# Kernel tuning notes

Hardware: AMD Instinct MI355X
Metric: run time of the kernel (lower is better)

The kernel has to match this reference:

```python
import jax, jax.numpy as jnp
import numpy as np

OFFSET_FP32 = np.uint32(1064828928)  # L-mul exponent-bias correction constant for float32


def lmul_matmul(A, B):
    """Approximate A @ B (m,n)x(n,p) via integer-add-as-multiply on float bit patterns.

    Torch ref adds bit patterns in int64 then truncates with .to(torch.uint32),
    i.e. arithmetic mod 2**32 -- identical to plain uint32 wraparound addition,
    so we stay in uint32 and avoid needing x64 mode.
    """
    Au = jax.lax.bitcast_convert_type(A, jnp.uint32)          # (m, n)
    Bu = jax.lax.bitcast_convert_type(B, jnp.uint32)          # (n, p)
    prod_bits = Au[:, :, None] + Bu[None, :, :] - OFFSET_FP32  # (m, n, p), wraps mod 2^32
    prod = jax.lax.bitcast_convert_type(prod_bits, jnp.float32)
    return prod.sum(axis=1)                                    # (m, p)


def setup_inputs() -> dict:
    key = jax.random.key(0)
    k1, k2, k3 = jax.random.split(key, 3)
    m, n, p = 256, 512, 512
    x = jax.random.normal(k1, (m, n), dtype=jnp.float32)
    bound = 1.0 / np.sqrt(n)  # kaiming_uniform(a=sqrt(5)) -> U(-1/sqrt(fan_in), 1/sqrt(fan_in))
    weight = jax.random.uniform(k2, (p, n), dtype=jnp.float32, minval=-bound, maxval=bound)
    bias = jax.random.uniform(k3, (p,), dtype=jnp.float32, minval=-bound, maxval=bound)
    return {"x": x, "weight": weight, "bias": bias}


def reference(x, weight, bias):
    out = lmul_matmul(x, weight.T)
    return out + bias
```

## Files before the change

kernel.cpp:

```cpp
#include <hip/hip_runtime.h>
#include <stdint.h>


#define OFFSET_FP32 1064828928u

constexpr int M = 256;
constexpr int N = 512;
constexpr int P = 512;

constexpr int BM = 8;
constexpr int BP = 64;
constexpr int TM = 4;

__global__ __launch_bounds__(512) void lmul_linear_kernel(
    const uint32_t* __restrict__ xb,
    const uint32_t* __restrict__ wb,
    const float*    __restrict__ bias,
    float*          __restrict__ out)
{
    __shared__ uint32_t Bs[BP][N];
    __shared__ float    Red[4][BM][BP];

    const int tid  = threadIdx.x;
    const int lane = tid & 63;
    const int wq   = __builtin_amdgcn_readfirstlane(tid >> 6);
    const int ks   = wq & 3;
    const int mq   = wq >> 2;

    const int p0 = blockIdx.y * BP;
    const int m0 = blockIdx.x * BM + mq * TM;

    auto stage = [&](int h) {
        #pragma unroll
        for (int i = 0; i < 8; ++i) {
            const int row = wq * 8 + i;
            const uint32_t* src = wb + (size_t)(p0 + row) * N
                                + (size_t)(h * 64 + (lane ^ (row & 7))) * 4;
            uint32_t* dst = &Bs[row][h * 256];
            __builtin_amdgcn_global_load_lds(
                (const __attribute__((address_space(1))) uint32_t*)src,
                (__attribute__((address_space(3))) uint32_t*)dst,
                16, 0, 0);
        }
    };

    float acc[TM][4] = {};
    const int rot = lane & 7;

    const uint32_t* xr0 = xb + (size_t)(m0 + 0) * N;
    const uint32_t* xr1 = xb + (size_t)(m0 + 1) * N;
    const uint32_t* xr2 = xb + (size_t)(m0 + 2) * N;
    const uint32_t* xr3 = xb + (size_t)(m0 + 3) * N;

    auto compute = [&](int h) {
        const uint32_t* brow = &Bs[lane][(h * 64 + ks * 16) * 4];
        const int xoff = h * 256 + ks * 64;
        #pragma unroll 8
        for (int j = 0; j < 16; ++j) {
            const uint4 b  = *(const uint4*)&brow[(j ^ rot) * 4];
            const uint4 a0 = *(const uint4*)(xr0 + xoff + j * 4);
            const uint4 a1 = *(const uint4*)(xr1 + xoff + j * 4);
            const uint4 a2 = *(const uint4*)(xr2 + xoff + j * 4);
            const uint4 a3 = *(const uint4*)(xr3 + xoff + j * 4);
            acc[0][0] += __uint_as_float((a0.x - OFFSET_FP32) + b.x);
            acc[0][1] += __uint_as_float((a0.y - OFFSET_FP32) + b.y);
            acc[0][2] += __uint_as_float((a0.z - OFFSET_FP32) + b.z);
            acc[0][3] += __uint_as_float((a0.w - OFFSET_FP32) + b.w);
            acc[1][0] += __uint_as_float((a1.x - OFFSET_FP32) + b.x);
            acc[1][1] += __uint_as_float((a1.y - OFFSET_FP32) + b.y);
            acc[1][2] += __uint_as_float((a1.z - OFFSET_FP32) + b.z);
            acc[1][3] += __uint_as_float((a1.w - OFFSET_FP32) + b.w);
            acc[2][0] += __uint_as_float((a2.x - OFFSET_FP32) + b.x);
            acc[2][1] += __uint_as_float((a2.y - OFFSET_FP32) + b.y);
            acc[2][2] += __uint_as_float((a2.z - OFFSET_FP32) + b.z);
            acc[2][3] += __uint_as_float((a2.w - OFFSET_FP32) + b.w);
            acc[3][0] += __uint_as_float((a3.x - OFFSET_FP32) + b.x);
            acc[3][1] += __uint_as_float((a3.y - OFFSET_FP32) + b.y);
            acc[3][2] += __uint_as_float((a3.z - OFFSET_FP32) + b.z);
            acc[3][3] += __uint_as_float((a3.w - OFFSET_FP32) + b.w);
        }
    };

    stage(0);
    __syncthreads();
    stage(1);
    compute(0);
    __syncthreads();
    compute(1);

    #pragma unroll
    for (int r = 0; r < TM; ++r)
        Red[ks][mq * TM + r][lane] =
            (acc[r][0] + acc[r][1]) + (acc[r][2] + acc[r][3]);
    __syncthreads();

    const int rr = tid >> 6;
    const int p  = p0 + lane;
    const float s = (Red[0][rr][lane] + Red[1][rr][lane])
                  + (Red[2][rr][lane] + Red[3][rr][lane]);
    out[(size_t)(blockIdx.x * BM + rr) * P + p] = s + bias[p];
}

extern "C" void kernel_launch(void* const* d_in, const int* in_sizes, int n_in,
                              void* d_out, int out_size, void* d_ws, size_t ws_size,
                              hipStream_t stream) {
    const uint32_t* xb   = (const uint32_t*)d_in[0];
    const uint32_t* wb   = (const uint32_t*)d_in[1];
    const float*    bias = (const float*)d_in[2];
    float*          out  = (float*)d_out;

    dim3 grid(M / BM, P / BP);
    dim3 block(512);
    lmul_linear_kernel<<<grid, block, 0, stream>>>(xb, wb, bias, out);
}
```

Before: 64.13 us.

## Stage x tile in LDS, pipeline weights in four quarters, use v_add3

After: 149.8 us. +133.6%, slower.

```diff
diff --git a/kernel.cpp b/kernel.cpp
--- a/kernel.cpp
+++ b/kernel.cpp
@@ -11,6 +11,14 @@
 constexpr int BM = 8;
 constexpr int BP = 64;
 constexpr int TM = 4;
+constexpr int NQ = 4;
+constexpr int QK = 128;
+
+__device__ __forceinline__ float lmul1(uint32_t a, uint32_t b, uint32_t negOff) {
+    uint32_t u;
+    asm("v_add3_u32 %0, %1, %2, %3" : "=v"(u) : "v"(a), "v"(b), "s"(negOff));
+    return __uint_as_float(u);
+}
 
 __global__ __launch_bounds__(512) void lmul_linear_kernel(
     const uint32_t* __restrict__ xb,
@@ -18,7 +26,8 @@
     const float*    __restrict__ bias,
     float*          __restrict__ out)
 {
-    __shared__ uint32_t Bs[BP][N];
+    __shared__ uint32_t Bs[NQ][BP][QK];
+    __shared__ uint32_t Xs[BM * N];
     __shared__ float    Red[4][BM][BP];
 
     const int tid  = threadIdx.x;
@@ -28,15 +37,15 @@
     const int mq   = wq >> 2;
 
     const int p0 = blockIdx.y * BP;
-    const int m0 = blockIdx.x * BM + mq * TM;
 
-    auto stage = [&](int h) {
+    auto stage_w = [&](int h) {
         #pragma unroll
-        for (int i = 0; i < 8; ++i) {
-            const int row = wq * 8 + i;
-            const uint32_t* src = wb + (size_t)(p0 + row) * N
-                                + (size_t)(h * 64 + (lane ^ (row & 7))) * 4;
-            uint32_t* dst = &Bs[row][h * 256];
+        for (int i = 0; i < 4; ++i) {
+            const int row = wq * 8 + i * 2 + (lane >> 5);
+            const int g   = lane & 31;
+            const uint32_t* src = wb + (size_t)(p0 + row) * N + h * QK
+                                     + (size_t)((g ^ (row & 7)) * 4);
+            uint32_t* dst = &Bs[h][wq * 8 + i * 2][0];
             __builtin_amdgcn_global_load_lds(
                 (const __attribute__((address_space(1))) uint32_t*)src,
                 (__attribute__((address_space(3))) uint32_t*)dst,
@@ -44,49 +53,61 @@
         }
     };
 
+    {
+        const uint32_t* xsrc = xb + (size_t)blockIdx.x * BM * N;
+        stage_w(0);
+        #pragma unroll
+        for (int i = 0; i < 2; ++i) {
+            const int call = wq * 2 + i;
+            const uint32_t* src = xsrc + call * 256 + lane * 4;
+            uint32_t* dst = &Xs[call * 256];
+            __builtin_amdgcn_global_load_lds(
+                (const __attribute__((address_space(1))) uint32_t*)src,
+                (__attribute__((address_space(3))) uint32_t*)dst,
+                16, 0, 0);
+        }
+    }
+
     float acc[TM][4] = {};
-    const int rot = lane & 7;
+    const int      rot     = lane & 7;
+    const uint32_t NEG_OFF = 0u - OFFSET_FP32;
 
-    const uint32_t* xr0 = xb + (size_t)(m0 + 0) * N;
-    const uint32_t* xr1 = xb + (size_t)(m0 + 1) * N;
-    const uint32_t* xr2 = xb + (size_t)(m0 + 2) * N;
-    const uint32_t* xr3 = xb + (size_t)(m0 + 3) * N;
+    __syncthreads();
 
-    auto compute = [&](int h) {
-        const uint32_t* brow = &Bs[lane][(h * 64 + ks * 16) * 4];
-        const int xoff = h * 256 + ks * 64;
-        #pragma unroll 8
-        for (int j = 0; j < 16; ++j) {
+    #pragma unroll
+    for (int h = 0; h < NQ; ++h) {
+        if (h + 1 < NQ) stage_w(h + 1);
+
+        const uint32_t* brow = &Bs[h][lane][ks * 32];
+        const uint32_t* xq   = &Xs[(mq * TM) * N + h * QK + ks * 32];
+
+        #pragma unroll
+        for (int j = 0; j < 8; ++j) {
             const uint4 b  = *(const uint4*)&brow[(j ^ rot) * 4];
-            const uint4 a0 = *(const uint4*)(xr0 + xoff + j * 4);
-            const uint4 a1 = *(const uint4*)(xr1 + xoff + j * 4);
-            const uint4 a2 = *(const uint4*)(xr2 + xoff + j * 4);
-            const uint4 a3 = *(const uint4*)(xr3 + xoff + j * 4);
-            acc[0][0] += __uint_as_float((a0.x - OFFSET_FP32) + b.x);
-            acc[0][1] += __uint_as_float((a0.y - OFFSET_FP32) + b.y);
-            acc[0][2] += __uint_as_float((a0.z - OFFSET_FP32) + b.z);
-            acc[0][3] += __uint_as_float((a0.w - OFFSET_FP32) + b.w);
-            acc[1][0] += __uint_as_float((a1.x - OFFSET_FP32) + b.x);
-            acc[1][1] += __uint_as_float((a1.y - OFFSET_FP32) + b.y);
-            acc[1][2] += __uint_as_float((a1.z - OFFSET_FP32) + b.z);
-            acc[1][3] += __uint_as_float((a1.w - OFFSET_FP32) + b.w);
-            acc[2][0] += __uint_as_float((a2.x - OFFSET_FP32) + b.x);
-            acc[2][1] += __uint_as_float((a2.y - OFFSET_FP32) + b.y);
-            acc[2][2] += __uint_as_float((a2.z - OFFSET_FP32) + b.z);
-            acc[2][3] += __uint_as_float((a2.w - OFFSET_FP32) + b.w);
-            acc[3][0] += __uint_as_float((a3.x - OFFSET_FP32) + b.x);
-            acc[3][1] += __uint_as_float((a3.y - OFFSET_FP32) + b.y);
-            acc[3][2] += __uint_as_float((a3.z - OFFSET_FP32) + b.z);
-            acc[3][3] += __uint_as_float((a3.w - OFFSET_FP32) + b.w);
+            const uint4 a0 = *(const uint4*)&xq[0 * N + j * 4];
+            const uint4 a1 = *(const uint4*)&xq[1 * N + j * 4];
+            const uint4 a2 = *(const uint4*)&xq[2 * N + j * 4];
+            const uint4 a3 = *(const uint4*)&xq[3 * N + j * 4];
+            acc[0][0] += lmul1(a0.x, b.x, NEG_OFF);
+            acc[0][1] += lmul1(a0.y, b.y, NEG_OFF);
+            acc[0][2] += lmul1(a0.z, b.z, NEG_OFF);
+            acc[0][3] += lmul1(a0.w, b.w, NEG_OFF);
+            acc[1][0] += lmul1(a1.x, b.x, NEG_OFF);
+            acc[1][1] += lmul1(a1.y, b.y, NEG_OFF);
+            acc[1][2] += lmul1(a1.z, b.z, NEG_OFF);
+            acc[1][3] += lmul1(a1.w, b.w, NEG_OFF);
+            acc[2][0] += lmul1(a2.x, b.x, NEG_OFF);
+            acc[2][1] += lmul1(a2.y, b.y, NEG_OFF);
+            acc[2][2] += lmul1(a2.z, b.z, NEG_OFF);
+            acc[2][3] += lmul1(a2.w, b.w, NEG_OFF);
+            acc[3][0] += lmul1(a3.x, b.x, NEG_OFF);
+            acc[3][1] += lmul1(a3.y, b.y, NEG_OFF);
+            acc[3][2] += lmul1(a3.z, b.z, NEG_OFF);
+            acc[3][3] += lmul1(a3.w, b.w, NEG_OFF);
         }
-    };
 
-    stage(0);
-    __syncthreads();
-    stage(1);
-    compute(0);
-    __syncthreads();
-    compute(1);
+        if (h + 1 < NQ) __syncthreads();
+    }
 
     #pragma unroll
     for (int r = 0; r < TM; ++r)
```
